# Performance work log

Hardware: AMD Instinct MI355X
Metric: run time of the kernel (lower is better)

Reference implementation:

```python
import jax, jax.numpy as jnp
import numpy as np

N_NODES = 50000
N_EDGES = 400000
NODE_DIM = 128
EDGE_DIM = 64
HIDDEN = 128  # must equal NODE_DIM (index_add into zeros_like(node_feat))
EPS = 1e-8


def _param(key, shape):
    fan_in = shape[0]
    return (jax.random.normal(key, shape, jnp.float32) / np.sqrt(fan_in)).astype(jnp.float32)


def setup_inputs() -> dict:
    key = jax.random.key(0)
    ks = jax.random.split(key, 20)
    inp = {
        'node_feat': jax.random.normal(ks[0], (N_NODES, NODE_DIM), jnp.float32),
        'edge_attr': jax.random.normal(ks[1], (N_EDGES, EDGE_DIM), jnp.float32),
        'coords': 5.0 * jax.random.normal(ks[2], (N_NODES, 3), jnp.float32),
        'edge_index': jax.random.randint(ks[3], (2, N_EDGES), 0, N_NODES, dtype=jnp.int32),
        # edge_mlp: Linear(2*node+edge -> hidden), SiLU, Linear(hidden -> hidden), SiLU
        'We1': _param(ks[4], (2 * NODE_DIM + EDGE_DIM, HIDDEN)),
        'be1': jnp.zeros((HIDDEN,), jnp.float32),
        'We2': _param(ks[5], (HIDDEN, HIDDEN)),
        'be2': jnp.zeros((HIDDEN,), jnp.float32),
        # node_mlp: Linear(node+hidden -> hidden), SiLU, Linear(hidden -> node)
        'Wn1': _param(ks[6], (NODE_DIM + HIDDEN, HIDDEN)),
        'bn1': jnp.zeros((HIDDEN,), jnp.float32),
        'Wn2': _param(ks[7], (HIDDEN, NODE_DIM)),
        'bn2': jnp.zeros((NODE_DIM,), jnp.float32),
        # coord_mlp: Linear(hidden -> hidden//2), SiLU, Linear(hidden//2 -> 1)
        'Wc1': _param(ks[8], (HIDDEN, HIDDEN // 2)),
        'bc1': jnp.zeros((HIDDEN // 2,), jnp.float32),
        'Wc2': _param(ks[9], (HIDDEN // 2, 1)),
        'bc2': jnp.zeros((1,), jnp.float32),
    }
    return inp


def reference(node_feat, edge_attr, coords, edge_index,
              We1, be1, We2, be2,
              Wn1, bn1, Wn2, bn2,
              Wc1, bc1, Wc2, bc2):
    src, dst = edge_index[0], edge_index[1]
    n_nodes = node_feat.shape[0]

    # gather -> edge MLP
    edge_feat = jnp.concatenate([node_feat[src], node_feat[dst], edge_attr], axis=-1)  # [E, 2*ND+ED]
    edge_message = jax.nn.silu(jax.nn.silu(edge_feat @ We1 + be1) @ We2 + be2)         # [E, H]

    # scatter-add messages to destination nodes
    aggr = jax.ops.segment_sum(edge_message, dst, num_segments=n_nodes)                # [N, H]

    # node update (residual)
    node_in = jnp.concatenate([node_feat, aggr], axis=-1)
    node_update = jax.nn.silu(node_in @ Wn1 + bn1) @ Wn2 + bn2
    updated_nodes = node_feat + node_update

    # equivariant coordinate update
    coord_w = jax.nn.silu(edge_message @ Wc1 + bc1) @ Wc2 + bc2                        # [E, 1]
    coord_diff = coords[src] - coords[dst]                                             # [E, 3]
    coord_diff = coord_diff / (jnp.linalg.norm(coord_diff, axis=-1, keepdims=True) + EPS)
    coord_update = jax.ops.segment_sum(coord_w * coord_diff, dst, num_segments=n_nodes)
    updated_coords = coords + coord_update

    return (updated_nodes, updated_coords)
```

## Files before the change

kernel.cpp:

```cpp
#include <hip/hip_runtime.h>
#include <hip/hip_bf16.h>
#include <math.h>
#include <stdint.h>

#define NN 50000
#define NE 400000

typedef __attribute__((ext_vector_type(8))) short short8;
typedef __attribute__((ext_vector_type(4))) float f32x4;

#define OFF_W1S  0
#define OFF_W1D  16384
#define OFF_W1E  32768
#define OFF_WE2T 40960
#define OFF_WN1T 57344
#define OFF_WN2T 90112
#define OFF_WC1T 106496
#define W_TOTAL  114688

#define NZ4 ((NN * 128 + NN * 3 + NN) / 4)

__device__ __forceinline__ float silu_f(float x) {
    return x * (1.0f / (1.0f + __expf(-x)));
}
__device__ __forceinline__ short f2bf(float f) {
    __hip_bfloat16 b = __float2bfloat16(f);
    return *reinterpret_cast<short*>(&b);
}
__device__ __forceinline__ float bf2f(short s) {
    uint32_t u = ((uint32_t)(uint16_t)s) << 16;
    float f; __builtin_memcpy(&f, &u, 4); return f;
}
__device__ __forceinline__ uint32_t pk2(float lo, float hi) {
    return (uint32_t)(uint16_t)f2bf(lo) | ((uint32_t)(uint16_t)f2bf(hi) << 16);
}
__device__ __forceinline__ short8 cvt8(float4 a, float4 b) {
    short8 r;
    r[0] = f2bf(a.x); r[1] = f2bf(a.y); r[2] = f2bf(a.z); r[3] = f2bf(a.w);
    r[4] = f2bf(b.x); r[5] = f2bf(b.y); r[6] = f2bf(b.z); r[7] = f2bf(b.w);
    return r;
}

__device__ __forceinline__ short8 exch8(uint32_t e0, uint32_t e1,
                                        uint32_t o0, uint32_t o1,
                                        int g, int le) {
    const int srcA = le + 16 * ((g & 1) * 2);
    const int srcB = srcA + 16;
    const uint32_t a0e = __shfl((int)e0, srcA), a0o = __shfl((int)o0, srcA);
    const uint32_t a1e = __shfl((int)e1, srcA), a1o = __shfl((int)o1, srcA);
    const uint32_t b0e = __shfl((int)e0, srcB), b0o = __shfl((int)o0, srcB);
    const uint32_t b1e = __shfl((int)e1, srcB), b1o = __shfl((int)o1, srcB);
    const bool hi = (g & 2) != 0;
    uint32_t v[4];
    v[0] = hi ? a0o : a0e;  v[1] = hi ? a1o : a1e;
    v[2] = hi ? b0o : b0e;  v[3] = hi ? b1o : b1e;
    short8 r; __builtin_memcpy(&r, v, 16); return r;
}

__global__ __launch_bounds__(256) void prep_kernel(
    const float* __restrict__ We1, const float* __restrict__ We2,
    const float* __restrict__ Wn1, const float* __restrict__ Wn2,
    const float* __restrict__ Wc1, short* __restrict__ wb,
    float4* __restrict__ zbase)
{
    const int i = blockIdx.x * 256 + threadIdx.x;
    if (i < W_TOTAL) {
        float v; int rel, n, k;
        if (i < OFF_W1D)       { rel = i;            n = rel >> 7; k = rel & 127; v = We1[k * 128 + n]; }
        else if (i < OFF_W1E)  { rel = i - OFF_W1D;  n = rel >> 7; k = rel & 127; v = We1[(k + 128) * 128 + n]; }
        else if (i < OFF_WE2T) { rel = i - OFF_W1E;  n = rel >> 6; k = rel & 63;  v = We1[(k + 256) * 128 + n]; }
        else if (i < OFF_WN1T) { rel = i - OFF_WE2T; n = rel >> 7; k = rel & 127; v = We2[k * 128 + n]; }
        else if (i < OFF_WN2T) { rel = i - OFF_WN1T; n = rel >> 8; k = rel & 255; v = Wn1[k * 128 + n]; }
        else if (i < OFF_WC1T) { rel = i - OFF_WN2T; n = rel >> 7; k = rel & 127; v = Wn2[k * 128 + n]; }
        else                   { rel = i - OFF_WC1T; n = rel >> 7; k = rel & 127; v = Wc1[k * 64 + n]; }
        wb[i] = f2bf(v);
    } else if (i < W_TOTAL + NZ4) {
        zbase[i - W_TOTAL] = make_float4(0.f, 0.f, 0.f, 0.f);
    }
}

__global__ __launch_bounds__(256) void hist_kernel(const int* __restrict__ ei, int* __restrict__ cnt) {
    const int e = blockIdx.x * 256 + threadIdx.x;
    if (e < NE) atomicAdd(&cnt[ei[NE + e]], 1);
}

__global__ __launch_bounds__(256) void scanA_kernel(const int* __restrict__ cnt,
                                                    int* __restrict__ eoff, int* __restrict__ bsum) {
    __shared__ int sm[256];
    const int t = threadIdx.x, idx = blockIdx.x * 256 + t;
    const int v = (idx < NN) ? cnt[idx] : 0;
    sm[t] = v; __syncthreads();
    #pragma unroll
    for (int o = 1; o < 256; o <<= 1) {
        const int x = (t >= o) ? sm[t - o] : 0;
        __syncthreads();
        sm[t] += x;
        __syncthreads();
    }
    if (idx < NN) eoff[idx] = sm[t] - v;
    if (t == 255) bsum[blockIdx.x] = sm[255];
}

__global__ __launch_bounds__(256) void scanB_kernel(const int* __restrict__ bsum,
                                                    int* __restrict__ bexcl, int nb) {
    __shared__ int sm[256];
    const int t = threadIdx.x;
    const int v = (t < nb) ? bsum[t] : 0;
    sm[t] = v; __syncthreads();
    #pragma unroll
    for (int o = 1; o < 256; o <<= 1) {
        const int x = (t >= o) ? sm[t - o] : 0;
        __syncthreads();
        sm[t] += x;
        __syncthreads();
    }
    bexcl[t] = sm[t] - v;
}

__global__ __launch_bounds__(256) void scanC_kernel(const int* __restrict__ eoff,
                                                    const int* __restrict__ bexcl,
                                                    int* __restrict__ cursor) {
    const int idx = blockIdx.x * 256 + threadIdx.x;
    if (idx < NN) cursor[idx] = eoff[idx] + bexcl[blockIdx.x];
}

__global__ __launch_bounds__(256) void fill_kernel(const int* __restrict__ ei,
                                                   int* __restrict__ cursor, int* __restrict__ csr) {
    const int e = blockIdx.x * 256 + threadIdx.x;
    if (e < NE) {
        const int pos = atomicAdd(&cursor[ei[NE + e]], 1);
        csr[pos] = e;
    }
}

__global__ __launch_bounds__(256, 4) void ynode_kernel(
    const float* __restrict__ nf, const short* __restrict__ wb,
    short* __restrict__ ysb, short* __restrict__ ydb)
{
    const int tid = threadIdx.x;
    const int wv = tid >> 6, lane = tid & 63, le = lane & 15, grp = lane >> 4;
    const int nb = blockIdx.x * 128, wbase = wv * 32;
    const int row0 = min(nb + wbase + le, NN - 1);
    const int row1 = min(nb + wbase + 16 + le, NN - 1);

    #pragma unroll 1
    for (int pass = 0; pass < 2; ++pass) {
        const short* wt = wb + (pass ? OFF_W1D : OFF_W1S);
        short* op = pass ? ydb : ysb;

        f32x4 acc[2][8];
        #pragma unroll
        for (int m = 0; m < 2; ++m)
            #pragma unroll
            for (int t = 0; t < 8; ++t) acc[m][t] = (f32x4){0.f, 0.f, 0.f, 0.f};

        #pragma unroll
        for (int kc = 0; kc < 4; ++kc) {
            const int gk = kc * 32 + grp * 8;
            const float* p0 = nf + (size_t)row0 * 128 + gk;
            const float* p1 = nf + (size_t)row1 * 128 + gk;
            const short8 a0 = cvt8(*(const float4*)p0, *(const float4*)(p0 + 4));
            const short8 a1 = cvt8(*(const float4*)p1, *(const float4*)(p1 + 4));
            short8 bfv[8];
            #pragma unroll
            for (int t = 0; t < 8; ++t)
                bfv[t] = *(const short8*)(wt + (size_t)(t * 16 + le) * 128 + gk);
            #pragma unroll
            for (int t = 0; t < 8; ++t) {
                acc[0][t] = __builtin_amdgcn_mfma_f32_16x16x32_bf16(a0, bfv[t], acc[0][t], 0, 0, 0);
                acc[1][t] = __builtin_amdgcn_mfma_f32_16x16x32_bf16(a1, bfv[t], acc[1][t], 0, 0, 0);
            }
        }
        #pragma unroll
        for (int t = 0; t < 8; ++t)
            #pragma unroll
            for (int m = 0; m < 2; ++m)
                #pragma unroll
                for (int r = 0; r < 4; ++r) {
                    const int row = nb + wbase + m * 16 + grp * 4 + r;
                    if (row < NN)
                        op[(size_t)row * 128 + t * 16 + le] = f2bf(acc[m][t][r]);
                }
    }
}

__global__ __launch_bounds__(256, 3) void edge_kernel(
    const short* __restrict__ ysb, const short* __restrict__ ydb,
    const float* __restrict__ ea, const float* __restrict__ coords,
    const int* __restrict__ ei, const int* __restrict__ csr,
    const short* __restrict__ wb,
    const float* __restrict__ be1, const float* __restrict__ be2,
    const float* __restrict__ bc1, const float* __restrict__ bc2,
    const float* __restrict__ Wc2f,
    float* __restrict__ aggr, float* __restrict__ coord_acc)
{
    __shared__ float Ht4[4][16 * 136];

    const int tid = threadIdx.x;
    const int wv = tid >> 6, lane = tid & 63, le = lane & 15, g = lane >> 4;
    const int base = (blockIdx.x * 4 + wv) * 32;
    float* Ht = Ht4[wv];

    const int eA = csr[base + le], eB = csr[base + 16 + le];
    const int sA = ei[eA], dA = ei[NE + eA];
    const int sB = ei[eB], dB = ei[NE + eB];

    short8 ysA[4], ydA[4], ysB[4], ydB8[4];
    #pragma unroll
    for (int cc = 0; cc < 4; ++cc) {
        ysA[cc]  = *(const short8*)(ysb + (size_t)sA * 128 + cc * 32 + g * 8);
        ydA[cc]  = *(const short8*)(ydb + (size_t)dA * 128 + cc * 32 + g * 8);
        ysB[cc]  = *(const short8*)(ysb + (size_t)sB * 128 + cc * 32 + g * 8);
        ydB8[cc] = *(const short8*)(ydb + (size_t)dB * 128 + cc * 32 + g * 8);
    }

    short8 eaA[2], eaB2[2];
    #pragma unroll
    for (int kc = 0; kc < 2; ++kc) {
        const float* pA = ea + (size_t)eA * 64 + kc * 32 + g * 8;
        const float* pB = ea + (size_t)eB * 64 + kc * 32 + g * 8;
        eaA[kc]  = cvt8(*(const float4*)pA, *(const float4*)(pA + 4));
        eaB2[kc] = cvt8(*(const float4*)pB, *(const float4*)(pB + 4));
    }

    f32x4 accA[8], accB[8];
    #pragma unroll
    for (int t = 0; t < 8; ++t) { accA[t] = (f32x4){0.f,0.f,0.f,0.f}; accB[t] = (f32x4){0.f,0.f,0.f,0.f}; }

    const short* w1e = wb + OFF_W1E;
    #pragma unroll
    for (int kc = 0; kc < 2; ++kc) {
        const int gk = kc * 32 + g * 8;
        short8 wfv[8];
        #pragma unroll
        for (int t = 0; t < 8; ++t)
            wfv[t] = *(const short8*)(w1e + (size_t)(t * 16 + le) * 64 + gk);
        #pragma unroll
        for (int t = 0; t < 8; ++t) {
            accA[t] = __builtin_amdgcn_mfma_f32_16x16x32_bf16(wfv[t], eaA[kc],  accA[t], 0, 0, 0);
            accB[t] = __builtin_amdgcn_mfma_f32_16x16x32_bf16(wfv[t], eaB2[kc], accB[t], 0, 0, 0);
        }
    }

    uint32_t hpA[8][2], hpB[8][2];
    #pragma unroll
    for (int t = 0; t < 8; ++t) {
        hpA[t][0] = pk2(accA[t][0], accA[t][1]);  hpA[t][1] = pk2(accA[t][2], accA[t][3]);
        hpB[t][0] = pk2(accB[t][0], accB[t][1]);  hpB[t][1] = pk2(accB[t][2], accB[t][3]);
    }

    short8 h1A[4], h1B[4];
    #pragma unroll
    for (int cc = 0; cc < 4; ++cc) {
        const short8 exA = exch8(hpA[cc*2][0], hpA[cc*2][1], hpA[cc*2+1][0], hpA[cc*2+1][1], g, le);
        const short8 exB = exch8(hpB[cc*2][0], hpB[cc*2][1], hpB[cc*2+1][0], hpB[cc*2+1][1], g, le);
        const float* bp = be1 + cc * 32 + g * 8;
        #pragma unroll
        for (int j = 0; j < 8; ++j) {
            h1A[cc][j] = f2bf(silu_f(bf2f(exA[j]) + bf2f(ysA[cc][j]) + bf2f(ydA[cc][j])  + bp[j]));
            h1B[cc][j] = f2bf(silu_f(bf2f(exB[j]) + bf2f(ysB[cc][j]) + bf2f(ydB8[cc][j]) + bp[j]));
        }
    }

    f32x4 a2A[8], a2B[8];
    #pragma unroll
    for (int t = 0; t < 8; ++t) { a2A[t] = (f32x4){0.f,0.f,0.f,0.f}; a2B[t] = (f32x4){0.f,0.f,0.f,0.f}; }

    const short* w2 = wb + OFF_WE2T;
    #pragma unroll
    for (int cc = 0; cc < 4; ++cc) {
        const int gk = cc * 32 + g * 8;
        short8 wfv[8];
        #pragma unroll
        for (int t = 0; t < 8; ++t)
            wfv[t] = *(const short8*)(w2 + (size_t)(t * 16 + le) * 128 + gk);
        #pragma unroll
        for (int t = 0; t < 8; ++t) {
            a2A[t] = __builtin_amdgcn_mfma_f32_16x16x32_bf16(wfv[t], h1A[cc], a2A[t], 0, 0, 0);
            a2B[t] = __builtin_amdgcn_mfma_f32_16x16x32_bf16(wfv[t], h1B[cc], a2B[t], 0, 0, 0);
        }
    }

    uint32_t hqA[8][2], hqB[8][2];
    #pragma unroll 1
    for (int ph = 0; ph < 2; ++ph) {
        const f32x4* a2 = ph ? a2B : a2A;
        const int dt = ph ? dB : dA;
        uint32_t (*hq)[2] = ph ? hqB : hqA;

        #pragma unroll
        for (int t = 0; t < 8; ++t) {
            float hv[4];
            #pragma unroll
            for (int r = 0; r < 4; ++r) {
                const int col = t * 16 + g * 4 + r;
                hv[r] = silu_f(a2[t][r] + be2[col]);
                Ht[le * 136 + col] = hv[r];
            }
            hq[t][0] = pk2(hv[0], hv[1]);
            hq[t][1] = pk2(hv[2], hv[3]);
        }

        const int c0 = g * 16 + le;
        const int c1 = c0 + 64;
        float a0 = 0.f, a1 = 0.f;
        int dprev = __shfl(dt, 0);
        #pragma unroll 1
        for (int row = 0; row < 16; ++row) {
            const int dr = __shfl(dt, row);
            if (dr != dprev) {
                atomicAdd(&aggr[(size_t)dprev * 128 + c0], a0);
                atomicAdd(&aggr[(size_t)dprev * 128 + c1], a1);
                a0 = 0.f; a1 = 0.f;
                dprev = dr;
            }
            a0 += Ht[row * 136 + c0];
            a1 += Ht[row * 136 + c1];
        }
        atomicAdd(&aggr[(size_t)dprev * 128 + c0], a0);
        atomicAdd(&aggr[(size_t)dprev * 128 + c1], a1);
    }

    short8 h2A[4], h2B[4];
    #pragma unroll
    for (int cc = 0; cc < 4; ++cc) {
        h2A[cc] = exch8(hqA[cc*2][0], hqA[cc*2][1], hqA[cc*2+1][0], hqA[cc*2+1][1], g, le);
        h2B[cc] = exch8(hqB[cc*2][0], hqB[cc*2][1], hqB[cc*2+1][0], hqB[cc*2+1][1], g, le);
    }

    f32x4 c3A[4], c3B[4];
    #pragma unroll
    for (int t = 0; t < 4; ++t) { c3A[t] = (f32x4){0.f,0.f,0.f,0.f}; c3B[t] = (f32x4){0.f,0.f,0.f,0.f}; }

    const short* wc = wb + OFF_WC1T;
    #pragma unroll
    for (int cc = 0; cc < 4; ++cc) {
        const int gk = cc * 32 + g * 8;
        short8 wfv[4];
        #pragma unroll
        for (int t = 0; t < 4; ++t)
            wfv[t] = *(const short8*)(wc + (size_t)(t * 16 + le) * 128 + gk);
        #pragma unroll
        for (int t = 0; t < 4; ++t) {
            c3A[t] = __builtin_amdgcn_mfma_f32_16x16x32_bf16(wfv[t], h2A[cc], c3A[t], 0, 0, 0);
            c3B[t] = __builtin_amdgcn_mfma_f32_16x16x32_bf16(wfv[t], h2B[cc], c3B[t], 0, 0, 0);
        }
    }

    float partA = 0.f, partB = 0.f;
    #pragma unroll
    for (int t = 0; t < 4; ++t)
        #pragma unroll
        for (int r = 0; r < 4; ++r) {
            const int col = t * 16 + g * 4 + r;
            const float bc = bc1[col], wv2 = Wc2f[col];
            partA += silu_f(c3A[t][r] + bc) * wv2;
            partB += silu_f(c3B[t][r] + bc) * wv2;
        }
    partA += __shfl_xor(partA, 16); partA += __shfl_xor(partA, 32);
    partB += __shfl_xor(partB, 16); partB += __shfl_xor(partB, 32);

    #pragma unroll 1
    for (int ph = 0; ph < 2; ++ph) {
        const int s0 = ph ? sB : sA, d0 = ph ? dB : dA;
        const float wq = (ph ? partB : partA) + bc2[0];
        const float dx = coords[3 * s0 + 0] - coords[3 * d0 + 0];
        const float dy = coords[3 * s0 + 1] - coords[3 * d0 + 1];
        const float dz = coords[3 * s0 + 2] - coords[3 * d0 + 2];
        const float inv = wq / (sqrtf(dx * dx + dy * dy + dz * dz) + 1e-8f);
        float vx = dx * inv, vy = dy * inv, vz = dz * inv;

        const int prevd = __shfl(d0, (le == 0) ? 0 : (le - 1));
        const bool head = (le == 0) || (prevd != d0);
        float sx = vx, sy = vy, sz = vz;
        #pragma unroll 1
        for (int j = 1; j < 16; ++j) {
            const float tx = __shfl(vx, le + j);
            const float ty = __shfl(vy, le + j);
            const float tz = __shfl(vz, le + j);
            const int dj = __shfl(d0, le + j);
            if ((le + j < 16) && (dj == d0)) { sx += tx; sy += ty; sz += tz; }
        }
        if (g == 0 && head) {
            atomicAdd(&coord_acc[3 * d0 + 0], sx);
            atomicAdd(&coord_acc[3 * d0 + 1], sy);
            atomicAdd(&coord_acc[3 * d0 + 2], sz);
        }
    }
}

__global__ __launch_bounds__(256, 3) void node_kernel(
    const float* __restrict__ nf, const float* __restrict__ coords,
    const short* __restrict__ wb,
    const float* __restrict__ bn1, const float* __restrict__ bn2,
    const float* __restrict__ aggr, const float* __restrict__ coord_acc,
    float* __restrict__ out)
{
    __shared__ short Hs[128][136];

    const int tid = threadIdx.x;
    const int wv = tid >> 6, lane = tid & 63, le = lane & 15, grp = lane >> 4;
    const int nb = blockIdx.x * 128, wbase = wv * 32;
    const int row0 = min(nb + wbase + le, NN - 1);
    const int row1 = min(nb + wbase + 16 + le, NN - 1);

    f32x4 acc[2][8];
    #pragma unroll
    for (int m = 0; m < 2; ++m)
        #pragma unroll
        for (int t = 0; t < 8; ++t) acc[m][t] = (f32x4){0.f, 0.f, 0.f, 0.f};

    const short* w1 = wb + OFF_WN1T;
    #pragma unroll
    for (int kc = 0; kc < 8; ++kc) {
        const int gk = kc * 32 + grp * 8;
        const float* p0 = (kc < 4) ? nf + (size_t)row0 * 128 + gk : aggr + (size_t)row0 * 128 + gk - 128;
        const float* p1 = (kc < 4) ? nf + (size_t)row1 * 128 + gk : aggr + (size_t)row1 * 128 + gk - 128;
        const short8 a0 = cvt8(*(const float4*)p0, *(const float4*)(p0 + 4));
        const short8 a1 = cvt8(*(const float4*)p1, *(const float4*)(p1 + 4));
        short8 bfv[8];
        #pragma unroll
        for (int t = 0; t < 8; ++t)
            bfv[t] = *(const short8*)(w1 + (size_t)(t * 16 + le) * 256 + gk);
        #pragma unroll
        for (int t = 0; t < 8; ++t) {
            acc[0][t] = __builtin_amdgcn_mfma_f32_16x16x32_bf16(a0, bfv[t], acc[0][t], 0, 0, 0);
            acc[1][t] = __builtin_amdgcn_mfma_f32_16x16x32_bf16(a1, bfv[t], acc[1][t], 0, 0, 0);
        }
    }
    #pragma unroll
    for (int t = 0; t < 8; ++t) {
        const float b1 = bn1[t * 16 + le];
        #pragma unroll
        for (int m = 0; m < 2; ++m)
            #pragma unroll
            for (int r = 0; r < 4; ++r)
                Hs[wbase + m * 16 + grp * 4 + r][t * 16 + le] = f2bf(silu_f(acc[m][t][r] + b1));
    }

    f32x4 acc2[2][8];
    #pragma unroll
    for (int m = 0; m < 2; ++m)
        #pragma unroll
        for (int t = 0; t < 8; ++t) acc2[m][t] = (f32x4){0.f, 0.f, 0.f, 0.f};

    const short* w2 = wb + OFF_WN2T;
    #pragma unroll
    for (int kc = 0; kc < 4; ++kc) {
        const int gk = kc * 32 + grp * 8;
        const short8 a0 = *(const short8*)&Hs[wbase + le][gk];
        const short8 a1 = *(const short8*)&Hs[wbase + 16 + le][gk];
        short8 bfv[8];
        #pragma unroll
        for (int t = 0; t < 8; ++t)
            bfv[t] = *(const short8*)(w2 + (size_t)(t * 16 + le) * 128 + gk);
        #pragma unroll
        for (int t = 0; t < 8; ++t) {
            acc2[0][t] = __builtin_amdgcn_mfma_f32_16x16x32_bf16(a0, bfv[t], acc2[0][t], 0, 0, 0);
            acc2[1][t] = __builtin_amdgcn_mfma_f32_16x16x32_bf16(a1, bfv[t], acc2[1][t], 0, 0, 0);
        }
    }
    #pragma unroll
    for (int t = 0; t < 8; ++t) {
        const float b2 = bn2[t * 16 + le];
        #pragma unroll
        for (int m = 0; m < 2; ++m)
            #pragma unroll
            for (int r = 0; r < 4; ++r) {
                const int row = nb + wbase + m * 16 + grp * 4 + r;
                if (row < NN) {
                    const int c = t * 16 + le;
                    out[(size_t)row * 128 + c] = acc2[m][t][r] + b2 + nf[(size_t)row * 128 + c];
                }
            }
    }

    for (int i = tid; i < 384; i += 256) {
        const int n = nb + i / 3, j = i % 3;
        if (n < NN)
            out[(size_t)NN * 128 + 3 * n + j] = coords[3 * n + j] + coord_acc[3 * n + j];
    }
}

extern "C" void kernel_launch(void* const* d_in, const int* in_sizes, int n_in,
                              void* d_out, int out_size, void* d_ws, size_t ws_size,
                              hipStream_t stream)
{
    const float* node_feat  = (const float*)d_in[0];
    const float* edge_attr  = (const float*)d_in[1];
    const float* coords     = (const float*)d_in[2];
    const int*   edge_index = (const int*)d_in[3];
    const float* We1 = (const float*)d_in[4];
    const float* be1 = (const float*)d_in[5];
    const float* We2 = (const float*)d_in[6];
    const float* be2 = (const float*)d_in[7];
    const float* Wn1 = (const float*)d_in[8];
    const float* bn1 = (const float*)d_in[9];
    const float* Wn2 = (const float*)d_in[10];
    const float* bn2 = (const float*)d_in[11];
    const float* Wc1 = (const float*)d_in[12];
    const float* bc1 = (const float*)d_in[13];
    const float* Wc2 = (const float*)d_in[14];
    const float* bc2 = (const float*)d_in[15];
    float* out = (float*)d_out;

    const size_t sz_wb  = (size_t)W_TOTAL * 2;
    const size_t sz_agg = (size_t)NN * 128 * 4;
    const size_t sz_cac = (size_t)NN * 3 * 4;
    const size_t sz_cnt = (size_t)NN * 4;
    const size_t sz_y   = (size_t)NN * 128 * 2;

    char* p = (char*)d_ws;
    short* wbf       = (short*)p;  p += sz_wb;
    float* aggr      = (float*)p;  p += sz_agg;
    float* coord_acc = (float*)p;  p += sz_cac;
    int*   cnt       = (int*)p;    p += sz_cnt;
    short* ysb       = (short*)p;  p += sz_y;
    short* ydb       = (short*)p;  p += sz_y;
    int*   eoff      = (int*)p;    p += (size_t)NN * 4;
    int*   bsum      = (int*)p;    p += 1024;
    int*   bexcl     = (int*)p;    p += 1024;
    int*   cursor    = (int*)p;    p += (size_t)NN * 4;
    int*   csr       = (int*)p;
    (void)ws_size;

    const int eg = NE / 128;
    const int ng = (NN + 127) / 128;
    const int eg256 = (NE + 255) / 256;
    const int sg = (NN + 255) / 256;
    const int pg = (W_TOTAL + NZ4 + 255) / 256;

    prep_kernel<<<pg, 256, 0, stream>>>(We1, We2, Wn1, Wn2, Wc1, wbf, (float4*)aggr);
    ynode_kernel<<<ng, 256, 0, stream>>>(node_feat, wbf, ysb, ydb);

    hist_kernel<<<eg256, 256, 0, stream>>>(edge_index, cnt);
    scanA_kernel<<<sg, 256, 0, stream>>>(cnt, eoff, bsum);
    scanB_kernel<<<1, 256, 0, stream>>>(bsum, bexcl, sg);
    scanC_kernel<<<sg, 256, 0, stream>>>(eoff, bexcl, cursor);
    fill_kernel<<<eg256, 256, 0, stream>>>(edge_index, cursor, csr);

    edge_kernel<<<eg, 256, 0, stream>>>(
        ysb, ydb, edge_attr, coords, edge_index, csr, wbf,
        be1, be2, bc1, bc2, Wc2, aggr, coord_acc);

    node_kernel<<<ng, 256, 0, stream>>>(
        node_feat, coords, wbf, bn1, bn2, aggr, coord_acc, out);
}
```

Baseline: 358.1 us.

## Replace atomic scatter with per-edge message buffer and CSR segmented sum

When the workspace is large enough, the edge kernel writes each edge's bf16 hidden message and weighted coordinate vector to per-edge buffers instead of doing atomic adds. A new kernel sums each node's CSR edge range into a bf16 aggregate and writes the final coordinates, and the node kernel reads that bf16 aggregate directly. This removes the float atomics, the zeroing of the large fp32 aggregate and the shared-memory staging in the edge kernel, and raises the edge kernel's occupancy bound. In exchange it writes and rereads a roughly 100 MB per-edge buffer and adds a kernel launch, and the fallback path is kept behind a workspace-size check.

```diff
diff --git a/kernel.cpp b/kernel.cpp
--- a/kernel.cpp
+++ b/kernel.cpp
@@ -17,8 +17,6 @@
 #define OFF_WN2T 90112
 #define OFF_WC1T 106496
 #define W_TOTAL  114688
-
-#define NZ4 ((NN * 128 + NN * 3 + NN) / 4)
 
 __device__ __forceinline__ float silu_f(float x) {
     return x * (1.0f / (1.0f + __expf(-x)));
@@ -61,7 +59,7 @@
     const float* __restrict__ We1, const float* __restrict__ We2,
     const float* __restrict__ Wn1, const float* __restrict__ Wn2,
     const float* __restrict__ Wc1, short* __restrict__ wb,
-    float4* __restrict__ zbase)
+    float4* __restrict__ zbase, int nz4)
 {
     const int i = blockIdx.x * 256 + threadIdx.x;
     if (i < W_TOTAL) {
@@ -74,7 +72,7 @@
         else if (i < OFF_WC1T) { rel = i - OFF_WN2T; n = rel >> 7; k = rel & 127; v = Wn2[k * 128 + n]; }
         else                   { rel = i - OFF_WC1T; n = rel >> 7; k = rel & 127; v = Wc1[k * 64 + n]; }
         wb[i] = f2bf(v);
-    } else if (i < W_TOTAL + NZ4) {
+    } else if (i < W_TOTAL + nz4) {
         zbase[i - W_TOTAL] = make_float4(0.f, 0.f, 0.f, 0.f);
     }
 }
@@ -117,11 +115,16 @@
     bexcl[t] = sm[t] - v;
 }
 
-__global__ __launch_bounds__(256) void scanC_kernel(const int* __restrict__ eoff,
+__global__ __launch_bounds__(256) void scanC_kernel(int* __restrict__ off,
                                                     const int* __restrict__ bexcl,
                                                     int* __restrict__ cursor) {
     const int idx = blockIdx.x * 256 + threadIdx.x;
-    if (idx < NN) cursor[idx] = eoff[idx] + bexcl[blockIdx.x];
+    if (idx < NN) {
+        const int o = off[idx] + bexcl[blockIdx.x];
+        off[idx] = o;
+        cursor[idx] = o;
+    }
+    if (idx == 0) off[NN] = NE;
 }
 
 __global__ __launch_bounds__(256) void fill_kernel(const int* __restrict__ ei,
@@ -184,7 +187,8 @@
     }
 }
 
-__global__ __launch_bounds__(256, 3) void edge_kernel(
+template<int MODE>
+__global__ __launch_bounds__(256, 4) void edge_kernel(
     const short* __restrict__ ysb, const short* __restrict__ ydb,
     const float* __restrict__ ea, const float* __restrict__ coords,
     const int* __restrict__ ei, const int* __restrict__ csr,
@@ -192,14 +196,15 @@
     const float* __restrict__ be1, const float* __restrict__ be2,
     const float* __restrict__ bc1, const float* __restrict__ bc2,
     const float* __restrict__ Wc2f,
+    short* __restrict__ h2b, float* __restrict__ cwv,
     float* __restrict__ aggr, float* __restrict__ coord_acc)
 {
-    __shared__ float Ht4[4][16 * 136];
+    extern __shared__ float HtDyn[];
 
     const int tid = threadIdx.x;
     const int wv = tid >> 6, lane = tid & 63, le = lane & 15, g = lane >> 4;
     const int base = (blockIdx.x * 4 + wv) * 32;
-    float* Ht = Ht4[wv];
+    float* Ht = HtDyn + wv * (16 * 136);
 
     const int eA = csr[base + le], eB = csr[base + 16 + le];
     const int sA = ei[eA], dA = ei[NE + eA];
@@ -282,43 +287,58 @@
     }
 
     uint32_t hqA[8][2], hqB[8][2];
-    #pragma unroll 1
-    for (int ph = 0; ph < 2; ++ph) {
-        const f32x4* a2 = ph ? a2B : a2A;
-        const int dt = ph ? dB : dA;
-        uint32_t (*hq)[2] = ph ? hqB : hqA;
-
+    if constexpr (MODE == 1) {
         #pragma unroll
         for (int t = 0; t < 8; ++t) {
             float hv[4];
             #pragma unroll
-            for (int r = 0; r < 4; ++r) {
-                const int col = t * 16 + g * 4 + r;
-                hv[r] = silu_f(a2[t][r] + be2[col]);
-                Ht[le * 136 + col] = hv[r];
+            for (int r = 0; r < 4; ++r) hv[r] = silu_f(a2A[t][r] + be2[t * 16 + g * 4 + r]);
+            hqA[t][0] = pk2(hv[0], hv[1]);  hqA[t][1] = pk2(hv[2], hv[3]);
+            uint32_t pr[2] = {hqA[t][0], hqA[t][1]};
+            __builtin_memcpy(h2b + (size_t)(base + le) * 128 + t * 16 + g * 4, pr, 8);
+            #pragma unroll
+            for (int r = 0; r < 4; ++r) hv[r] = silu_f(a2B[t][r] + be2[t * 16 + g * 4 + r]);
+            hqB[t][0] = pk2(hv[0], hv[1]);  hqB[t][1] = pk2(hv[2], hv[3]);
+            uint32_t qr[2] = {hqB[t][0], hqB[t][1]};
+            __builtin_memcpy(h2b + (size_t)(base + 16 + le) * 128 + t * 16 + g * 4, qr, 8);
+        }
+    } else {
+        #pragma unroll 1
+        for (int ph = 0; ph < 2; ++ph) {
+            const f32x4* a2 = ph ? a2B : a2A;
+            const int dt = ph ? dB : dA;
+            uint32_t (*hq)[2] = ph ? hqB : hqA;
+            #pragma unroll
+            for (int t = 0; t < 8; ++t) {
+                float hv[4];
+                #pragma unroll
+                for (int r = 0; r < 4; ++r) {
+                    const int col = t * 16 + g * 4 + r;
+                    hv[r] = silu_f(a2[t][r] + be2[col]);
+                    Ht[le * 136 + col] = hv[r];
+                }
+                hq[t][0] = pk2(hv[0], hv[1]);
+                hq[t][1] = pk2(hv[2], hv[3]);
             }
-            hq[t][0] = pk2(hv[0], hv[1]);
-            hq[t][1] = pk2(hv[2], hv[3]);
-        }
-
-        const int c0 = g * 16 + le;
-        const int c1 = c0 + 64;
-        float a0 = 0.f, a1 = 0.f;
-        int dprev = __shfl(dt, 0);
-        #pragma unroll 1
-        for (int row = 0; row < 16; ++row) {
-            const int dr = __shfl(dt, row);
-            if (dr != dprev) {
-                atomicAdd(&aggr[(size_t)dprev * 128 + c0], a0);
-                atomicAdd(&aggr[(size_t)dprev * 128 + c1], a1);
-                a0 = 0.f; a1 = 0.f;
-                dprev = dr;
+            const int c0 = g * 16 + le;
+            const int c1 = c0 + 64;
+            float a0 = 0.f, a1 = 0.f;
+            int dprev = __shfl(dt, 0);
+            #pragma unroll 1
+            for (int row = 0; row < 16; ++row) {
+                const int dr = __shfl(dt, row);
+                if (dr != dprev) {
+                    atomicAdd(&aggr[(size_t)dprev * 128 + c0], a0);
+                    atomicAdd(&aggr[(size_t)dprev * 128 + c1], a1);
+                    a0 = 0.f; a1 = 0.f;
+                    dprev = dr;
+                }
+                a0 += Ht[row * 136 + c0];
+                a1 += Ht[row * 136 + c1];
             }
-            a0 += Ht[row * 136 + c0];
-            a1 += Ht[row * 136 + c1];
-        }
-        atomicAdd(&aggr[(size_t)dprev * 128 + c0], a0);
-        atomicAdd(&aggr[(size_t)dprev * 128 + c1], a1);
+            atomicAdd(&aggr[(size_t)dprev * 128 + c0], a0);
+            atomicAdd(&aggr[(size_t)dprev * 128 + c1], a1);
+        }
     }
 
     short8 h2A[4], h2B[4];
@@ -360,40 +380,93 @@
     partA += __shfl_xor(partA, 16); partA += __shfl_xor(partA, 32);
     partB += __shfl_xor(partB, 16); partB += __shfl_xor(partB, 32);
 
-    #pragma unroll 1
-    for (int ph = 0; ph < 2; ++ph) {
-        const int s0 = ph ? sB : sA, d0 = ph ? dB : dA;
-        const float wq = (ph ? partB : partA) + bc2[0];
-        const float dx = coords[3 * s0 + 0] - coords[3 * d0 + 0];
-        const float dy = coords[3 * s0 + 1] - coords[3 * d0 + 1];
-        const float dz = coords[3 * s0 + 2] - coords[3 * d0 + 2];
-        const float inv = wq / (sqrtf(dx * dx + dy * dy + dz * dz) + 1e-8f);
-        float vx = dx * inv, vy = dy * inv, vz = dz * inv;
-
-        const int prevd = __shfl(d0, (le == 0) ? 0 : (le - 1));
-        const bool head = (le == 0) || (prevd != d0);
-        float sx = vx, sy = vy, sz = vz;
+    if constexpr (MODE == 1) {
+        if (g == 0) {
+            const float wq = partA + bc2[0];
+            const float dx = coords[3 * sA + 0] - coords[3 * dA + 0];
+            const float dy = coords[3 * sA + 1] - coords[3 * dA + 1];
+            const float dz = coords[3 * sA + 2] - coords[3 * dA + 2];
+            const float inv = wq / (sqrtf(dx * dx + dy * dy + dz * dz) + 1e-8f);
+            float* o = cwv + (size_t)(base + le) * 3;
+            o[0] = dx * inv; o[1] = dy * inv; o[2] = dz * inv;
+        } else if (g == 1) {
+            const float wq = partB + bc2[0];
+            const float dx = coords[3 * sB + 0] - coords[3 * dB + 0];
+            const float dy = coords[3 * sB + 1] - coords[3 * dB + 1];
+            const float dz = coords[3 * sB + 2] - coords[3 * dB + 2];
+            const float inv = wq / (sqrtf(dx * dx + dy * dy + dz * dz) + 1e-8f);
+            float* o = cwv + (size_t)(base + 16 + le) * 3;
+            o[0] = dx * inv; o[1] = dy * inv; o[2] = dz * inv;
+        }
+    } else {
         #pragma unroll 1
-        for (int j = 1; j < 16; ++j) {
-            const float tx = __shfl(vx, le + j);
-            const float ty = __shfl(vy, le + j);
-            const float tz = __shfl(vz, le + j);
-            const int dj = __shfl(d0, le + j);
-            if ((le + j < 16) && (dj == d0)) { sx += tx; sy += ty; sz += tz; }
-        }
-        if (g == 0 && head) {
-            atomicAdd(&coord_acc[3 * d0 + 0], sx);
-            atomicAdd(&coord_acc[3 * d0 + 1], sy);
-            atomicAdd(&coord_acc[3 * d0 + 2], sz);
-        }
-    }
-}
-
+        for (int ph = 0; ph < 2; ++ph) {
+            const int s0 = ph ? sB : sA, d0 = ph ? dB : dA;
+            const float wq = (ph ? partB : partA) + bc2[0];
+            const float dx = coords[3 * s0 + 0] - coords[3 * d0 + 0];
+            const float dy = coords[3 * s0 + 1] - coords[3 * d0 + 1];
+            const float dz = coords[3 * s0 + 2] - coords[3 * d0 + 2];
+            const float inv = wq / (sqrtf(dx * dx + dy * dy + dz * dz) + 1e-8f);
+            float vx = dx * inv, vy = dy * inv, vz = dz * inv;
+
+            const int prevd = __shfl(d0, (le == 0) ? 0 : (le - 1));
+            const bool head = (le == 0) || (prevd != d0);
+            float sx = vx, sy = vy, sz = vz;
+            #pragma unroll 1
+            for (int j = 1; j < 16; ++j) {
+                const float tx = __shfl(vx, le + j);
+                const float ty = __shfl(vy, le + j);
+                const float tz = __shfl(vz, le + j);
+                const int dj = __shfl(d0, le + j);
+                if ((le + j < 16) && (dj == d0)) { sx += tx; sy += ty; sz += tz; }
+            }
+            if (g == 0 && head) {
+                atomicAdd(&coord_acc[3 * d0 + 0], sx);
+                atomicAdd(&coord_acc[3 * d0 + 1], sy);
+                atomicAdd(&coord_acc[3 * d0 + 2], sz);
+            }
+        }
+    }
+}
+
+__global__ __launch_bounds__(256, 4) void aggrsum_kernel(
+    const short* __restrict__ h2b, const float* __restrict__ cwv,
+    const int* __restrict__ off, const float* __restrict__ coords,
+    short* __restrict__ aggrb, float* __restrict__ out)
+{
+    const int tid = threadIdx.x;
+    const int l16 = tid & 15, grp = tid >> 4;
+    const int n = blockIdx.x * 16 + grp;
+    if (n >= NN) return;
+
+    const int o0 = off[n], o1 = off[n + 1];
+    float s[8];
+    #pragma unroll
+    for (int j = 0; j < 8; ++j) s[j] = 0.f;
+    for (int i = o0; i < o1; ++i) {
+        const short8 v = *(const short8*)(h2b + (size_t)i * 128 + l16 * 8);
+        #pragma unroll
+        for (int j = 0; j < 8; ++j) s[j] += bf2f(v[j]);
+    }
+    short8 r;
+    #pragma unroll
+    for (int j = 0; j < 8; ++j) r[j] = f2bf(s[j]);
+    *(short8*)(aggrb + (size_t)n * 128 + l16 * 8) = r;
+
+    if (l16 < 3) {
+        float c = 0.f;
+        for (int i = o0; i < o1; ++i) c += cwv[(size_t)i * 3 + l16];
+        out[(size_t)NN * 128 + 3 * n + l16] = coords[3 * n + l16] + c;
+    }
+}
+
+template<int MODE>
 __global__ __launch_bounds__(256, 3) void node_kernel(
     const float* __restrict__ nf, const float* __restrict__ coords,
     const short* __restrict__ wb,
     const float* __restrict__ bn1, const float* __restrict__ bn2,
-    const float* __restrict__ aggr, const float* __restrict__ coord_acc,
+    const float* __restrict__ aggr, const short* __restrict__ aggrb,
+    const float* __restrict__ coord_acc,
     float* __restrict__ out)
 {
     __shared__ short Hs[128][136];
@@ -414,10 +487,21 @@
     #pragma unroll
     for (int kc = 0; kc < 8; ++kc) {
         const int gk = kc * 32 + grp * 8;
-        const float* p0 = (kc < 4) ? nf + (size_t)row0 * 128 + gk : aggr + (size_t)row0 * 128 + gk - 128;
-        const float* p1 = (kc < 4) ? nf + (size_t)row1 * 128 + gk : aggr + (size_t)row1 * 128 + gk - 128;
-        const short8 a0 = cvt8(*(const float4*)p0, *(const float4*)(p0 + 4));
-        const short8 a1 = cvt8(*(const float4*)p1, *(const float4*)(p1 + 4));
+        short8 a0, a1;
+        if (kc < 4) {
+            const float* p0 = nf + (size_t)row0 * 128 + gk;
+            const float* p1 = nf + (size_t)row1 * 128 + gk;
+            a0 = cvt8(*(const float4*)p0, *(const float4*)(p0 + 4));
+            a1 = cvt8(*(const float4*)p1, *(const float4*)(p1 + 4));
+        } else if constexpr (MODE == 1) {
+            a0 = *(const short8*)(aggrb + (size_t)row0 * 128 + gk - 128);
+            a1 = *(const short8*)(aggrb + (size_t)row1 * 128 + gk - 128);
+        } else {
+            const float* p0 = aggr + (size_t)row0 * 128 + gk - 128;
+            const float* p1 = aggr + (size_t)row1 * 128 + gk - 128;
+            a0 = cvt8(*(const float4*)p0, *(const float4*)(p0 + 4));
+            a1 = cvt8(*(const float4*)p1, *(const float4*)(p1 + 4));
+        }
         short8 bfv[8];
         #pragma unroll
         for (int t = 0; t < 8; ++t)
@@ -475,10 +559,12 @@
             }
     }
 
-    for (int i = tid; i < 384; i += 256) {
-        const int n = nb + i / 3, j = i % 3;
-        if (n < NN)
-            out[(size_t)NN * 128 + 3 * n + j] = coords[3 * n + j] + coord_acc[3 * n + j];
+    if constexpr (MODE == 0) {
+        for (int i = tid; i < 384; i += 256) {
+            const int n = nb + i / 3, j = i % 3;
+            if (n < NN)
+                out[(size_t)NN * 128 + 3 * n + j] = coords[3 * n + j] + coord_acc[3 * n + j];
+        }
     }
 }
 
@@ -504,45 +590,81 @@
     const float* bc2 = (const float*)d_in[15];
     float* out = (float*)d_out;
 
-    const size_t sz_wb  = (size_t)W_TOTAL * 2;
-    const size_t sz_agg = (size_t)NN * 128 * 4;
-    const size_t sz_cac = (size_t)NN * 3 * 4;
-    const size_t sz_cnt = (size_t)NN * 4;
-    const size_t sz_y   = (size_t)NN * 128 * 2;
-
-    char* p = (char*)d_ws;
-    short* wbf       = (short*)p;  p += sz_wb;
-    float* aggr      = (float*)p;  p += sz_agg;
-    float* coord_acc = (float*)p;  p += sz_cac;
-    int*   cnt       = (int*)p;    p += sz_cnt;
-    short* ysb       = (short*)p;  p += sz_y;
-    short* ydb       = (short*)p;  p += sz_y;
-    int*   eoff      = (int*)p;    p += (size_t)NN * 4;
-    int*   bsum      = (int*)p;    p += 1024;
-    int*   bexcl     = (int*)p;    p += 1024;
-    int*   cursor    = (int*)p;    p += (size_t)NN * 4;
-    int*   csr       = (int*)p;
-    (void)ws_size;
-
     const int eg = NE / 128;
     const int ng = (NN + 127) / 128;
     const int eg256 = (NE + 255) / 256;
     const int sg = (NN + 255) / 256;
-    const int pg = (W_TOTAL + NZ4 + 255) / 256;
-
-    prep_kernel<<<pg, 256, 0, stream>>>(We1, We2, Wn1, Wn2, Wc1, wbf, (float4*)aggr);
-    ynode_kernel<<<ng, 256, 0, stream>>>(node_feat, wbf, ysb, ydb);
-
-    hist_kernel<<<eg256, 256, 0, stream>>>(edge_index, cnt);
-    scanA_kernel<<<sg, 256, 0, stream>>>(cnt, eoff, bsum);
-    scanB_kernel<<<1, 256, 0, stream>>>(bsum, bexcl, sg);
-    scanC_kernel<<<sg, 256, 0, stream>>>(eoff, bexcl, cursor);
-    fill_kernel<<<eg256, 256, 0, stream>>>(edge_index, cursor, csr);
-
-    edge_kernel<<<eg, 256, 0, stream>>>(
-        ysb, ydb, edge_attr, coords, edge_index, csr, wbf,
-        be1, be2, bc1, bc2, Wc2, aggr, coord_acc);
-
-    node_kernel<<<ng, 256, 0, stream>>>(
-        node_feat, coords, wbf, bn1, bn2, aggr, coord_acc, out);
-}
+
+    const size_t sz_wb  = (size_t)W_TOTAL * 2;
+    const size_t sz_y   = (size_t)NN * 128 * 2;
+
+    const size_t need_stream = sz_wb + (size_t)NN * 4 + (size_t)(NN + 1) * 4 + 2048
+                             + (size_t)NE * 4 + 2 * sz_y + (size_t)NE * 12
+                             + (size_t)NE * 128 * 2;
+
+    if (ws_size >= need_stream) {
+        char* p = (char*)d_ws;
+        short* wbf    = (short*)p;  p += sz_wb;
+        int*   cnt    = (int*)p;    p += (size_t)NN * 4;
+        int*   off    = (int*)p;    p += (size_t)(NN + 1) * 4;
+        int*   bsum   = (int*)p;    p += 1024;
+        int*   bexcl  = (int*)p;    p += 1024;
+        int*   csr    = (int*)p;    p += (size_t)NE * 4;
+        short* ysb    = (short*)p;  p += sz_y;
+        short* ydb    = (short*)p;  p += sz_y;
+        float* cwv    = (float*)p;  p += (size_t)NE * 12;
+        short* h2b    = (short*)p;
+        short* aggrb  = ysb;
+
+        const int nz4 = NN / 4;
+        prep_kernel<<<(W_TOTAL + NN / 4 + 255) / 256, 256, 0, stream>>>(
+            We1, We2, Wn1, Wn2, Wc1, wbf, (float4*)cnt, nz4);
+        ynode_kernel<<<ng, 256, 0, stream>>>(node_feat, wbf, ysb, ydb);
+
+        hist_kernel<<<eg256, 256, 0, stream>>>(edge_index, cnt);
+        scanA_kernel<<<sg, 256, 0, stream>>>(cnt, off, bsum);
+        scanB_kernel<<<1, 256, 0, stream>>>(bsum, bexcl, sg);
+        scanC_kernel<<<sg, 256, 0, stream>>>(off, bexcl, cnt);
+        fill_kernel<<<eg256, 256, 0, stream>>>(edge_index, cnt, csr);
+
+        edge_kernel<1><<<eg, 256, 0, stream>>>(
+            ysb, ydb, edge_attr, coords, edge_index, csr, wbf,
+            be1, be2, bc1, bc2, Wc2, h2b, cwv, nullptr, nullptr);
+
+        aggrsum_kernel<<<(NN + 15) / 16, 256, 0, stream>>>(
+            h2b, cwv, off, coords, aggrb, out);
+
+        node_kernel<1><<<ng, 256, 0, stream>>>(
+            node_feat, coords, wbf, bn1, bn2, nullptr, aggrb, nullptr, out);
+    } else {
+        char* p = (char*)d_ws;
+        short* wbf       = (short*)p;  p += sz_wb;
+        float* aggr      = (float*)p;  p += (size_t)NN * 128 * 4;
+        float* coord_acc = (float*)p;  p += (size_t)NN * 3 * 4;
+        int*   cnt       = (int*)p;    p += (size_t)NN * 4;
+        short* ysb       = (short*)p;  p += sz_y;
+        short* ydb       = (short*)p;  p += sz_y;
+        int*   off       = (int*)p;    p += (size_t)(NN + 1) * 4;
+        int*   bsum      = (int*)p;    p += 1024;
+        int*   bexcl     = (int*)p;    p += 1024;
+        int*   csr       = (int*)p;
+
+        const int nz4 = (NN * 128 + NN * 3 + NN) / 4;
+        prep_kernel<<<(W_TOTAL + nz4 + 255) / 256, 256, 0, stream>>>(
+            We1, We2, Wn1, Wn2, Wc1, wbf, (float4*)aggr, nz4);
+        ynode_kernel<<<ng, 256, 0, stream>>>(node_feat, wbf, ysb, ydb);
+
+        hist_kernel<<<eg256, 256, 0, stream>>>(edge_index, cnt);
+        scanA_kernel<<<sg, 256, 0, stream>>>(cnt, off, bsum);
+        scanB_kernel<<<1, 256, 0, stream>>>(bsum, bexcl, sg);
+        scanC_kernel<<<sg, 256, 0, stream>>>(off, bexcl, cnt);
+        fill_kernel<<<eg256, 256, 0, stream>>>(edge_index, cnt, csr);
+
+        edge_kernel<0><<<eg, 256, 4 * 16 * 136 * 4, stream>>>(
+            ysb, ydb, edge_attr, coords, edge_index, csr, wbf,
+            be1, be2, bc1, bc2, Wc2, nullptr, nullptr, aggr, coord_acc);
+
+        node_kernel<0><<<ng, 256, 0, stream>>>(
+            node_feat, coords, wbf, bn1, bn2, aggr, nullptr, coord_acc, out);
+    }
+}
```

After: 468.7 us. 30.9% more time.
